# Performance work log

Measured on AMD Instinct MI355X. Metric: run time of the kernel, lower is better.

The kernel has to match this reference:

```python
import jax, jax.numpy as jnp
import numpy as np

B, N, K, OUT = 8, 2048, 30, 13


def _knn_idx(x, k):
    # x: [B,N,F] -> indices of k nearest neighbors (squared L2, includes self)
    sq = jnp.sum(x * x, axis=-1)  # [B,N]
    d = sq[:, :, None] + sq[:, None, :] - 2.0 * jnp.einsum('bnf,bmf->bnm', x, x)
    _, idx = jax.lax.top_k(-d, k)  # [B,N,k]
    return idx


def _edge_conv(x, W1, b1, g, be, W2, b2, k):
    # DynamicEdgeConv: kNN on feature space, message = MLP([x_i, x_j - x_i]), max aggr
    idx = _knn_idx(x, k)                                  # [B,N,k] (non-differentiable)
    xj = jax.vmap(lambda xb, ib: xb[ib])(x, idx)          # gather neighbors [B,N,k,F]
    xi = x[:, :, None, :]
    e = jnp.concatenate([jnp.broadcast_to(xi, xj.shape), xj - xi], axis=-1)  # [B,N,k,2F]
    # PyG MLP([2F,64,64]): Linear + BN(eval: affine) + ReLU, then plain Linear
    h = jax.nn.relu((e @ W1 + b1) * g + be)
    h = h @ W2 + b2
    return jnp.max(h, axis=2)                             # max over k neighbors -> [B,N,64]


def setup_inputs():
    key = jax.random.key(0)
    ks = jax.random.split(key, 40)

    def lin(i, fin, fout):
        W = jax.random.normal(ks[i], (fin, fout), jnp.float32) / np.sqrt(fin)
        return W, jnp.zeros((fout,), jnp.float32)

    inp = {}
    inp['x'] = jax.random.normal(ks[0], (B, N, 3), jnp.float32)
    inp['pos'] = jax.random.normal(ks[1], (B, N, 3), jnp.float32)
    inp['batch'] = jnp.repeat(jnp.arange(B, dtype=jnp.int32), N)
    i = 2
    for name, fin in [('c1', 12), ('c2', 128), ('c3', 128)]:
        W1, b1 = lin(i, fin, 64); i += 1
        W2, b2 = lin(i, 64, 64); i += 1
        inp[name + '_W1'] = W1; inp[name + '_b1'] = b1
        inp[name + '_g'] = 1.0 + 0.1 * jax.random.normal(ks[i], (64,), jnp.float32); i += 1
        inp[name + '_be'] = 0.1 * jax.random.normal(ks[i], (64,), jnp.float32); i += 1
        inp[name + '_W2'] = W2; inp[name + '_b2'] = b2
    dims = [192, 1024, 256, 128, OUT]
    for j in range(4):
        W, b = lin(i, dims[j], dims[j + 1]); i += 1
        inp[f'm_W{j + 1}'] = W; inp[f'm_b{j + 1}'] = b
    return inp


def reference(x, pos, batch,
              c1_W1, c1_b1, c1_g, c1_be, c1_W2, c1_b2,
              c2_W1, c2_b1, c2_g, c2_be, c2_W2, c2_b2,
              c3_W1, c3_b1, c3_g, c3_be, c3_W2, c3_b2,
              m_W1, m_b1, m_W2, m_b2, m_W3, m_b3, m_W4, m_b4):
    x0 = jnp.concatenate([pos, x], axis=-1)               # [B,N,6]
    x1 = _edge_conv(x0, c1_W1, c1_b1, c1_g, c1_be, c1_W2, c1_b2, K)
    x2 = _edge_conv(x1, c2_W1, c2_b1, c2_g, c2_be, c2_W2, c2_b2, K)
    x3 = _edge_conv(x2, c3_W1, c3_b1, c3_g, c3_be, c3_W2, c3_b2, K)
    h = jnp.concatenate([x1, x2, x3], axis=-1)            # [B,N,192]
    # classifier MLP([192,1024,256,128,OUT], norm=None): Linear+ReLU(+dropout=eval id), plain last
    h = jax.nn.relu(h @ m_W1 + m_b1)
    h = jax.nn.relu(h @ m_W2 + m_b2)
    h = jax.nn.relu(h @ m_W3 + m_b3)
    out = h @ m_W4 + m_b4
    return jax.nn.log_softmax(out, axis=-1), x3
```

## Files before the change

### kernel.cpp

```cpp
#include <hip/hip_runtime.h>

using u16 = unsigned short;
using u32 = unsigned int;
typedef short s8v __attribute__((ext_vector_type(8)));
typedef float f4v __attribute__((ext_vector_type(4)));

#define DEV static __device__ __forceinline__

DEV void cvt_split(float f, u16& h, u16& l) {
  u32 x = __builtin_bit_cast(u32, f);
  u32 rh = (x + 0x7FFFu + ((x >> 16) & 1u)) & 0xFFFF0000u;
  h = (u16)(rh >> 16);
  float fl = f - __builtin_bit_cast(float, rh);
  u32 y = __builtin_bit_cast(u32, fl);
  l = (u16)((y + 0x7FFFu + ((y >> 16) & 1u)) >> 16);
}

__global__ void k_misc0(const float* __restrict__ x, const float* __restrict__ pos,
                        float* __restrict__ x0, float* __restrict__ sq,
                        const float* __restrict__ W2c3, u16* __restrict__ eW2h, u16* __restrict__ eW2l) {
  int b = blockIdx.x;
  if (b < 64) {
    int p = b * 256 + threadIdx.x;
    float* o = x0 + (size_t)p * 8;
    float o0 = pos[p*3+0], o1 = pos[p*3+1], o2 = pos[p*3+2];
    float o3 = x[p*3+0],   o4 = x[p*3+1],   o5 = x[p*3+2];
    o[0] = o0; o[1] = o1; o[2] = o2;
    o[3] = o3; o[4] = o4; o[5] = o5;
    o[6] = 0.f; o[7] = 0.f;
    float s = ((o0*o0 + o4*o4) + (o2*o2 + 0.f)) + ((o1*o1 + o5*o5) + (o3*o3 + 0.f));
    sq[p] = s;
  } else {
    int e = (b - 64) * 256 + threadIdx.x;
    int k = e >> 6, n = e & 63;
    u16 h, l;
    cvt_split(W2c3[e], h, l);
    eW2h[n*72 + k] = h;
    eW2l[n*72 + k] = l;
  }
}

__global__ void k_splitmlp(const float* __restrict__ W1, const float* __restrict__ W2,
                           const float* __restrict__ W3,
                           u16* __restrict__ m1h, u16* __restrict__ m1l,
                           u16* __restrict__ m2h, u16* __restrict__ m2l,
                           u16* __restrict__ m3h, u16* __restrict__ m3l) {
  int b = blockIdx.x;
  u16 h, l;
  if (b < 768) {
    int e = b * 256 + threadIdx.x;
    if (e < 192 * 1024) {
      int k = e >> 10, n = e & 1023;
      cvt_split(W1[e], h, l);
      m1h[(size_t)n*200 + k] = h; m1l[(size_t)n*200 + k] = l;
    }
  } else if (b < 1792) {
    int e = (b - 768) * 256 + threadIdx.x;
    int k = e >> 8, n = e & 255;
    cvt_split(W2[e], h, l);
    m2h[(size_t)n*1032 + k] = h; m2l[(size_t)n*1032 + k] = l;
  } else {
    int e = (b - 1792) * 256 + threadIdx.x;
    int k = e >> 7, n = e & 127;
    cvt_split(W3[e], h, l);
    m3h[(size_t)n*264 + k] = h; m3l[(size_t)n*264 + k] = l;
  }
}

__global__ void k_splita(const float* __restrict__ A, u16* __restrict__ Ah, u16* __restrict__ Al) {
  int e = blockIdx.x * 256 + threadIdx.x;
  u16 h, l;
  cvt_split(A[e], h, l);
  Ah[e] = h; Al[e] = l;
}

template<int F>
__global__ __launch_bounds__(256, 2) void k_dist(const float* __restrict__ x, int stride,
    const float* __restrict__ sq, int cbase, float* __restrict__ D) {
  constexpr int PAD = F + 4;
  __shared__ __align__(16) float Xi[128 * PAD];
  __shared__ __align__(16) float Xj[128 * PAD];
  __shared__ float SQI[128], SQJ[128];
  int b  = blockIdx.z;
  int i0 = cbase + blockIdx.y * 128;
  int j0 = blockIdx.x * 128;
  int tid = threadIdx.x;
  constexpr int NPASS = 128 * (F / 4) / 256;
  #pragma unroll
  for (int ps = 0; ps < NPASS; ++ps) {
    int e4 = ps * 256 + tid;
    int r = e4 / (F / 4), f4 = (e4 % (F / 4)) * 4;
    *(float4*)&Xi[r*PAD + f4] = *(const float4*)&x[(size_t)(b*2048 + i0 + r)*stride + f4];
    *(float4*)&Xj[r*PAD + f4] = *(const float4*)&x[(size_t)(b*2048 + j0 + r)*stride + f4];
  }
  if (tid < 128) {
    SQI[tid] = sq[b*2048 + i0 + tid];
    SQJ[tid] = sq[b*2048 + j0 + tid];
  }
  __syncthreads();
  int tx = tid & 15, ty = tid >> 4;
  float acc[8][8];
  #pragma unroll
  for (int i = 0; i < 8; ++i)
    #pragma unroll
    for (int j = 0; j < 8; ++j) acc[i][j] = 0.f;
  #pragma unroll 2
  for (int kf = 0; kf < F; kf += 4) {
    float4 av[8], wv[8];
    #pragma unroll
    for (int i = 0; i < 8; ++i) av[i] = *(const float4*)&Xi[(ty + 16*i)*PAD + kf];
    #pragma unroll
    for (int j = 0; j < 8; ++j) wv[j] = *(const float4*)&Xj[(tx + 16*j)*PAD + kf];
    #pragma unroll
    for (int i = 0; i < 8; ++i)
      #pragma unroll
      for (int j = 0; j < 8; ++j) {
        acc[i][j] += av[i].x * wv[j].x;
        acc[i][j] += av[i].y * wv[j].y;
        acc[i][j] += av[i].z * wv[j].z;
        acc[i][j] += av[i].w * wv[j].w;
      }
  }
  #pragma unroll
  for (int i = 0; i < 8; ++i) {
    int row = ty + 16*i;
    float si = SQI[row];
    #pragma unroll
    for (int j = 0; j < 8; ++j) {
      int col = tx + 16*j;
      D[(size_t)(b*512 + blockIdx.y*128 + row)*2048 + j0 + col] =
          si + SQJ[col] - 2.f * acc[i][j];
    }
  }
}

__global__ __launch_bounds__(256) void k_topk(const float* __restrict__ D, int cbase,
                                              int* __restrict__ knn) {
  int wid  = blockIdx.x * 4 + (threadIdx.x >> 6);
  int lane = threadIdx.x & 63;
  int b = wid >> 9, il = wid & 511;
  const float* row = D + (size_t)(b*512 + il) * 2048;
  float v[32];
  #pragma unroll
  for (int s = 0; s < 32; ++s) v[s] = row[lane + 64*s];
  const float INFV = __builtin_bit_cast(float, 0x7f800000u);
  int wj = 0;
  #pragma unroll 1
  for (int it = 0; it < 30; ++it) {
    float mv = v[0]; int ms = 0;
    #pragma unroll
    for (int s = 1; s < 32; ++s) {
      bool lt = v[s] < mv;
      mv = lt ? v[s] : mv;
      ms = lt ? s : ms;
    }
    int mj = lane + (ms << 6);
    #pragma unroll
    for (int m = 1; m < 64; m <<= 1) {
      float ov = __shfl_xor(mv, m);
      int   oj = __shfl_xor(mj, m);
      bool take = (ov < mv) || ((ov == mv) && (oj < mj));
      mv = take ? ov : mv;
      mj = take ? oj : mj;
    }
    int gj = __builtin_amdgcn_readfirstlane(mj);
    if (lane == it) wj = gj;
    int owner = gj & 63, slot = gj >> 6;
    #pragma unroll
    for (int s = 0; s < 32; ++s) {
      if (slot == s) {
        if (lane == owner) v[s] = INFV;
      }
    }
  }
  if (lane < 30) knn[(size_t)(b*2048 + cbase + il)*30 + lane] = b*2048 + wj;
}

__global__ __launch_bounds__(256, 4) void k_prep(const float* __restrict__ x, int stride, int F,
    const float* __restrict__ W1, const float* __restrict__ b1,
    float* __restrict__ A0, float* __restrict__ V) {
  int p = blockIdx.x * 4 + (threadIdx.x >> 6);
  int lane = threadIdx.x & 63;
  float u = 0.f, v = 0.f;
  for (int f = 0; f < F; ++f) {
    float xv = x[(size_t)p*stride + f];
    float wa = W1[f*64 + lane];
    float wb = W1[(F + f)*64 + lane];
    u += xv * (wa - wb);
    v += xv * wb;
  }
  A0[p*64 + lane] = u + b1[lane];
  V[p*64 + lane]  = v;
}

__global__ __launch_bounds__(256, 3) void k_edge_b(const float* __restrict__ A0,
    const float* __restrict__ V, const int* __restrict__ knn,
    const float* __restrict__ W2, const float* __restrict__ b2,
    const float* __restrict__ g, const float* __restrict__ be,
    float* __restrict__ out, int ostride, float* __restrict__ sqout) {
  __shared__ __align__(16) float h1s[4][30][68];
  int wave = threadIdx.x >> 6, lane = threadIdx.x & 63;
  int p = blockIdx.x * 4 + wave;

  float a0 = A0[(size_t)p*64 + lane];
  float gg = g[lane], bbe = be[lane];
  const int* kr = knn + (size_t)p*30;

  #pragma unroll 2
  for (int k = 0; k < 30; ++k) {
    int j = kr[k];
    float v = V[(size_t)j*64 + lane];
    float pre = (a0 + v) * gg + bbe;
    h1s[wave][k][lane] = pre > 0.f ? pre : 0.f;
  }

  float w2c[64];
  #pragma unroll
  for (int c = 0; c < 64; ++c) w2c[c] = W2[c*64 + lane];

  float m = -3.0e38f;
  #pragma unroll 1
  for (int k = 0; k < 30; ++k) {
    float s0 = 0.f, s1 = 0.f, s2 = 0.f, s3 = 0.f;
    #pragma unroll
    for (int c = 0; c < 64; c += 4) {
      float4 hv = *(const float4*)&h1s[wave][k][c];
      s0 += hv.x * w2c[c+0];
      s1 += hv.y * w2c[c+1];
      s2 += hv.z * w2c[c+2];
      s3 += hv.w * w2c[c+3];
    }
    float h2 = (s0 + s1) + (s2 + s3);
    m = m > h2 ? m : h2;
  }
  float ov = m + b2[lane];
  out[(size_t)p*ostride + lane] = ov;

  float s = ov * ov;
  #pragma unroll
  for (int mm = 32; mm; mm >>= 1) s += __shfl_xor(s, mm);
  if (lane == 0) sqout[p] = s;
}

__global__ __launch_bounds__(256) void k_edge_m(const float* __restrict__ A0,
    const float* __restrict__ V, const int* __restrict__ knn,
    const u16* __restrict__ W2h, const u16* __restrict__ W2l,
    const float* __restrict__ b2,
    const float* __restrict__ g, const float* __restrict__ be,
    float* __restrict__ out, int ostride) {
  constexpr int PKW = 72;
  int p = blockIdx.x * 4 + (threadIdx.x >> 6);
  int lane = threadIdx.x & 63;
  int lr = lane & 15, kb = lane >> 4;

  const int* kr = knn + (size_t)p * 30;
  int j0 = kr[lr];
  int j1 = kr[lr + 16 < 30 ? lr + 16 : 29];

  s8v bh[4][2], bl[4][2];
  #pragma unroll
  for (int jf = 0; jf < 4; ++jf) {
    int n = jf*16 + lr;
    #pragma unroll
    for (int ks = 0; ks < 2; ++ks) {
      bh[jf][ks] = *(const s8v*)&W2h[n*PKW + ks*32 + kb*8];
      bl[jf][ks] = *(const s8v*)&W2l[n*PKW + ks*32 + kb*8];
    }
  }

  float base[2][8], gs[2][8];
  #pragma unroll
  for (int ks = 0; ks < 2; ++ks) {
    int cb = ks*32 + kb*8;
    float4 a0 = *(const float4*)&A0[(size_t)p*64 + cb];
    float4 a1 = *(const float4*)&A0[(size_t)p*64 + cb + 4];
    float4 g0 = *(const float4*)&g[cb];
    float4 g1 = *(const float4*)&g[cb + 4];
    float4 e0 = *(const float4*)&be[cb];
    float4 e1 = *(const float4*)&be[cb + 4];
    base[ks][0]=a0.x*g0.x+e0.x; base[ks][1]=a0.y*g0.y+e0.y;
    base[ks][2]=a0.z*g0.z+e0.z; base[ks][3]=a0.w*g0.w+e0.w;
    base[ks][4]=a1.x*g1.x+e1.x; base[ks][5]=a1.y*g1.y+e1.y;
    base[ks][6]=a1.z*g1.z+e1.z; base[ks][7]=a1.w*g1.w+e1.w;
    gs[ks][0]=g0.x; gs[ks][1]=g0.y; gs[ks][2]=g0.z; gs[ks][3]=g0.w;
    gs[ks][4]=g1.x; gs[ks][5]=g1.y; gs[ks][6]=g1.z; gs[ks][7]=g1.w;
  }

  s8v ah[2][2], al[2][2];
  #pragma unroll
  for (int mt = 0; mt < 2; ++mt) {
    const float* vr = V + (size_t)(mt ? j1 : j0) * 64;
    #pragma unroll
    for (int ks = 0; ks < 2; ++ks) {
      int cb = ks*32 + kb*8;
      float4 v0 = *(const float4*)&vr[cb];
      float4 v1 = *(const float4*)&vr[cb + 4];
      float hv[8];
      hv[0]=base[ks][0]+v0.x*gs[ks][0]; hv[1]=base[ks][1]+v0.y*gs[ks][1];
      hv[2]=base[ks][2]+v0.z*gs[ks][2]; hv[3]=base[ks][3]+v0.w*gs[ks][3];
      hv[4]=base[ks][4]+v1.x*gs[ks][4]; hv[5]=base[ks][5]+v1.y*gs[ks][5];
      hv[6]=base[ks][6]+v1.z*gs[ks][6]; hv[7]=base[ks][7]+v1.w*gs[ks][7];
      s8v hfrag, lfrag;
      #pragma unroll
      for (int e = 0; e < 8; ++e) {
        float h1 = hv[e] > 0.f ? hv[e] : 0.f;
        u16 hh, ll;
        cvt_split(h1, hh, ll);
        hfrag[e] = (short)hh; lfrag[e] = (short)ll;
      }
      ah[mt][ks] = hfrag; al[mt][ks] = lfrag;
    }
  }

  f4v acc[2][4];
  #pragma unroll
  for (int mt = 0; mt < 2; ++mt)
    #pragma unroll
    for (int jf = 0; jf < 4; ++jf) acc[mt][jf] = (f4v)(0.f);

  #pragma unroll
  for (int mt = 0; mt < 2; ++mt)
    #pragma unroll
    for (int jf = 0; jf < 4; ++jf)
      #pragma unroll
      for (int ks = 0; ks < 2; ++ks) {
        acc[mt][jf] = __builtin_amdgcn_mfma_f32_16x16x32_bf16(ah[mt][ks], bh[jf][ks], acc[mt][jf], 0, 0, 0);
        acc[mt][jf] = __builtin_amdgcn_mfma_f32_16x16x32_bf16(ah[mt][ks], bl[jf][ks], acc[mt][jf], 0, 0, 0);
        acc[mt][jf] = __builtin_amdgcn_mfma_f32_16x16x32_bf16(al[mt][ks], bh[jf][ks], acc[mt][jf], 0, 0, 0);
      }

  #pragma unroll
  for (int jf = 0; jf < 4; ++jf) {
    float m = fmaxf(fmaxf(acc[0][jf][0], acc[0][jf][1]), fmaxf(acc[0][jf][2], acc[0][jf][3]));
    float m1 = fmaxf(fmaxf(acc[1][jf][0], acc[1][jf][1]), fmaxf(acc[1][jf][2], acc[1][jf][3]));
    m = fmaxf(m, m1);
    m = fmaxf(m, __shfl_xor(m, 16));
    m = fmaxf(m, __shfl_xor(m, 32));
    if (kb == 0) out[(size_t)p*ostride + jf*16 + lr] = m + b2[jf*16 + lr];
  }
}

template<int NJF, int SPLIT>
__global__ __launch_bounds__(256) void k_mlp(
    const u16* __restrict__ Ahg, const u16* __restrict__ Alg, int lka,
    const u16* __restrict__ Wth, const u16* __restrict__ Wtl, int PKW,
    const float* __restrict__ bg,
    float* __restrict__ Cf, u16* __restrict__ Ch, u16* __restrict__ Cl,
    int ldc, int K) {
  int tid  = threadIdx.x;
  int wave = tid >> 6, lane = tid & 63;
  int wm = (wave >> 1) * 64, wn = (wave & 1) * (NJF*16);
  int lr = lane & 15, kb = lane >> 4;
  int m0 = blockIdx.y * 128, n0 = blockIdx.x * (2*NJF*16);

  f4v acc[4][NJF];
  #pragma unroll
  for (int i = 0; i < 4; ++i)
    #pragma unroll
    for (int j = 0; j < NJF; ++j) acc[i][j] = (f4v)(0.f);

  for (int k0 = 0; k0 < K; k0 += 32) {
    s8v bh[NJF], bl[NJF], ah[4], al[4];
    #pragma unroll
    for (int jf = 0; jf < NJF; ++jf) {
      int n = n0 + wn + jf*16 + lr;
      bh[jf] = *(const s8v*)&Wth[(size_t)n*PKW + k0 + kb*8];
      bl[jf] = *(const s8v*)&Wtl[(size_t)n*PKW + k0 + kb*8];
    }
    #pragma unroll
    for (int mf = 0; mf < 4; ++mf) {
      size_t a = (size_t)(m0 + wm + mf*16 + lr)*lka + k0 + kb*8;
      ah[mf] = *(const s8v*)&Ahg[a];
      al[mf] = *(const s8v*)&Alg[a];
    }
    #pragma unroll
    for (int mf = 0; mf < 4; ++mf)
      #pragma unroll
      for (int jf = 0; jf < NJF; ++jf) {
        acc[mf][jf] = __builtin_amdgcn_mfma_f32_16x16x32_bf16(ah[mf], bh[jf], acc[mf][jf], 0, 0, 0);
        acc[mf][jf] = __builtin_amdgcn_mfma_f32_16x16x32_bf16(ah[mf], bl[jf], acc[mf][jf], 0, 0, 0);
        acc[mf][jf] = __builtin_amdgcn_mfma_f32_16x16x32_bf16(al[mf], bh[jf], acc[mf][jf], 0, 0, 0);
      }
  }

  #pragma unroll
  for (int jf = 0; jf < NJF; ++jf) {
    int n = n0 + wn + jf*16 + lr;
    float bb = bg[n];
    #pragma unroll
    for (int mf = 0; mf < 4; ++mf) {
      #pragma unroll
      for (int r = 0; r < 4; ++r) {
        int m = m0 + wm + mf*16 + kb*4 + r;
        float v = acc[mf][jf][r] + bb;
        v = v > 0.f ? v : 0.f;
        if (SPLIT) {
          u16 h, l;
          cvt_split(v, h, l);
          Ch[(size_t)m*ldc + n] = h;
          Cl[(size_t)m*ldc + n] = l;
        } else {
          Cf[(size_t)m*ldc + n] = v;
        }
      }
    }
  }
}

__global__ __launch_bounds__(256) void k_head(const float* __restrict__ H3,
    const float* __restrict__ W4, const float* __restrict__ b4,
    float* __restrict__ out0, int pbase) {
  __shared__ float w4s[128 * 13];
  __shared__ float b4s[13];
  for (int e = threadIdx.x; e < 128*13; e += 256) w4s[e] = W4[e];
  if (threadIdx.x < 13) b4s[threadIdx.x] = b4[threadIdx.x];
  __syncthreads();
  int pl = blockIdx.x * 256 + threadIdx.x;
  float acc[13];
  #pragma unroll
  for (int c = 0; c < 13; ++c) acc[c] = b4s[c];
  const float* hr = H3 + (size_t)pl * 128;
  #pragma unroll 1
  for (int k = 0; k < 128; k += 4) {
    float4 h = *(const float4*)&hr[k];
    #pragma unroll
    for (int c = 0; c < 13; ++c) {
      acc[c] += h.x * w4s[(k+0)*13 + c];
      acc[c] += h.y * w4s[(k+1)*13 + c];
      acc[c] += h.z * w4s[(k+2)*13 + c];
      acc[c] += h.w * w4s[(k+3)*13 + c];
    }
  }
  float mx = acc[0];
  #pragma unroll
  for (int c = 1; c < 13; ++c) mx = fmaxf(mx, acc[c]);
  float s = 0.f;
  #pragma unroll
  for (int c = 0; c < 13; ++c) s += expf(acc[c] - mx);
  float lg = logf(s);
  size_t ob = (size_t)(pbase + pl) * 13;
  #pragma unroll
  for (int c = 0; c < 13; ++c) out0[ob + c] = acc[c] - mx - lg;
}

__global__ void k_out1(const float* __restrict__ hcat, float* __restrict__ out1) {
  int e = blockIdx.x * 256 + threadIdx.x;
  int p = e >> 6, c = e & 63;
  out1[e] = hcat[(size_t)p*192 + 128 + c];
}

extern "C" void kernel_launch(void* const* d_in, const int* in_sizes, int n_in,
                              void* d_out, int out_size, void* d_ws, size_t ws_size,
                              hipStream_t stream) {
  (void)in_sizes; (void)n_in; (void)out_size; (void)ws_size;
  const float* x   = (const float*)d_in[0];
  const float* pos = (const float*)d_in[1];
  const float* cw[3][6];
  for (int c = 0; c < 3; ++c)
    for (int t = 0; t < 6; ++t)
      cw[c][t] = (const float*)d_in[3 + c*6 + t];
  const float *mW[4], *mb[4];
  for (int j = 0; j < 4; ++j) {
    mW[j] = (const float*)d_in[21 + 2*j];
    mb[j] = (const float*)d_in[22 + 2*j];
  }

  float* ws   = (float*)d_ws;
  float* x0   = ws;
  float* sq   = x0 + 131072;
  int*   knn  = (int*)(sq + 16384);
  float* A0   = (float*)(knn + 491520);
  float* V    = A0 + 1048576;
  float* hcat = V + 1048576;
  float* U    = hcat + 3145728;
  float* H2c  = U + 8388608;
  float* H3c  = H2c + 2097152;
  u16*   eW2  = (u16*)(H3c + 1048576);

  u16* mwp = (u16*)(V + 524288);
  u16* m1h = mwp;            u16* m1l = m1h + 204800;
  u16* m2h = m1l + 204800;   u16* m2l = m2h + 264192;
  u16* m3h = m2l + 264192;   u16* m3l = m3h + 33792;
  u16* Aih = (u16*)A0;
  u16* Ail = Aih + 1572864;
  u16* H1h = (u16*)U;        u16* H1l = H1h + 8388608;
  u16* H2h = (u16*)H2c;      u16* H2l = H2h + 2097152;

  float* out0 = (float*)d_out;
  float* out1 = out0 + 8*2048*13;

  k_misc0<<<80, 256, 0, stream>>>(x, pos, x0, sq, cw[2][4], eW2, eW2 + 4608);

  for (int c = 0; c < 3; ++c) {
    const float* xin; int stride, F;
    if (c == 0)      { xin = x0;        stride = 8;   F = 6;  }
    else if (c == 1) { xin = hcat;      stride = 192; F = 64; }
    else             { xin = hcat + 64; stride = 192; F = 64; }
    for (int ch = 0; ch < 4; ++ch) {
      if (c == 0) k_dist<8> <<<dim3(16,4,8), 256, 0, stream>>>(xin, stride, sq, ch*512, U);
      else        k_dist<64><<<dim3(16,4,8), 256, 0, stream>>>(xin, stride, sq, ch*512, U);
      k_topk<<<1024, 256, 0, stream>>>(U, ch*512, knn);
    }
    k_prep<<<4096, 256, 0, stream>>>(xin, stride, F, cw[c][0], cw[c][1], A0, V);
    if (c < 2)
      k_edge_b<<<4096, 256, 0, stream>>>(A0, V, knn, cw[c][4], cw[c][5],
                                         cw[c][2], cw[c][3], hcat + 64*c, 192, sq);
    else
      k_edge_m<<<4096, 256, 0, stream>>>(A0, V, knn, eW2, eW2 + 4608,
                                         cw[c][5], cw[c][2], cw[c][3], hcat + 64*c, 192);
  }

  k_splitmlp<<<1920, 256, 0, stream>>>(mW[0], mW[1], mW[2], m1h, m1l, m2h, m2l, m3h, m3l);

  for (int ch = 0; ch < 2; ++ch) {
    k_splita<<<6144, 256, 0, stream>>>(hcat + (size_t)ch * 8192 * 192, Aih, Ail);
    k_mlp<4,1><<<dim3(8,64), 256, 0, stream>>>(Aih, Ail, 192,  m1h, m1l, 200,  mb[0],
                                               nullptr, H1h, H1l, 1024, 192);
    k_mlp<2,1><<<dim3(4,64), 256, 0, stream>>>(H1h, H1l, 1024, m2h, m2l, 1032, mb[1],
                                               nullptr, H2h, H2l, 256, 1024);
    k_mlp<2,0><<<dim3(2,64), 256, 0, stream>>>(H2h, H2l, 256,  m3h, m3l, 264,  mb[2],
                                               H3c, nullptr, nullptr, 128, 256);
    k_head<<<32, 256, 0, stream>>>(H3c, mW[3], mb[3], out0, ch*8192);
  }
  k_out1<<<4096, 256, 0, stream>>>(hcat, out1);
}
```

Baseline: 1.447 ms.

## Chunk k_dist feature loads, drop launch bound hints, precompute W1 difference

```diff
diff --git a/kernel.cpp b/kernel.cpp
--- a/kernel.cpp
+++ b/kernel.cpp
@@ -18,7 +18,10 @@
 
 __global__ void k_misc0(const float* __restrict__ x, const float* __restrict__ pos,
                         float* __restrict__ x0, float* __restrict__ sq,
-                        const float* __restrict__ W2c3, u16* __restrict__ eW2h, u16* __restrict__ eW2l) {
+                        const float* __restrict__ W2c3, u16* __restrict__ eW2h, u16* __restrict__ eW2l,
+                        const float* __restrict__ W1c1, const float* __restrict__ W1c2,
+                        const float* __restrict__ W1c3,
+                        float* __restrict__ wd1, float* __restrict__ wd2, float* __restrict__ wd3) {
   int b = blockIdx.x;
   if (b < 64) {
     int p = b * 256 + threadIdx.x;
@@ -30,13 +33,19 @@
     o[6] = 0.f; o[7] = 0.f;
     float s = ((o0*o0 + o4*o4) + (o2*o2 + 0.f)) + ((o1*o1 + o5*o5) + (o3*o3 + 0.f));
     sq[p] = s;
-  } else {
+  } else if (b < 80) {
     int e = (b - 64) * 256 + threadIdx.x;
     int k = e >> 6, n = e & 63;
     u16 h, l;
     cvt_split(W2c3[e], h, l);
     eW2h[n*72 + k] = h;
     eW2l[n*72 + k] = l;
+  } else if (b == 80) {
+    for (int e = threadIdx.x; e < 6*64; e += 256) wd1[e] = W1c1[e] - W1c1[6*64 + e];
+  } else if (b == 81) {
+    for (int e = threadIdx.x; e < 64*64; e += 256) wd2[e] = W1c2[e] - W1c2[64*64 + e];
+  } else {
+    for (int e = threadIdx.x; e < 64*64; e += 256) wd3[e] = W1c3[e] - W1c3[64*64 + e];
   }
 }
 
@@ -75,9 +84,10 @@
 }
 
 template<int F>
-__global__ __launch_bounds__(256, 2) void k_dist(const float* __restrict__ x, int stride,
+__global__ __launch_bounds__(256) void k_dist(const float* __restrict__ x, int stride,
     const float* __restrict__ sq, int cbase, float* __restrict__ D) {
-  constexpr int PAD = F + 4;
+  constexpr int BK = (F > 32) ? 32 : F;
+  constexpr int PAD = BK + 4;
   __shared__ __align__(16) float Xi[128 * PAD];
   __shared__ __align__(16) float Xj[128 * PAD];
   __shared__ float SQI[128], SQJ[128];
@@ -85,41 +95,45 @@
   int i0 = cbase + blockIdx.y * 128;
   int j0 = blockIdx.x * 128;
   int tid = threadIdx.x;
-  constexpr int NPASS = 128 * (F / 4) / 256;
-  #pragma unroll
-  for (int ps = 0; ps < NPASS; ++ps) {
-    int e4 = ps * 256 + tid;
-    int r = e4 / (F / 4), f4 = (e4 % (F / 4)) * 4;
-    *(float4*)&Xi[r*PAD + f4] = *(const float4*)&x[(size_t)(b*2048 + i0 + r)*stride + f4];
-    *(float4*)&Xj[r*PAD + f4] = *(const float4*)&x[(size_t)(b*2048 + j0 + r)*stride + f4];
-  }
   if (tid < 128) {
     SQI[tid] = sq[b*2048 + i0 + tid];
     SQJ[tid] = sq[b*2048 + j0 + tid];
   }
-  __syncthreads();
   int tx = tid & 15, ty = tid >> 4;
   float acc[8][8];
   #pragma unroll
   for (int i = 0; i < 8; ++i)
     #pragma unroll
     for (int j = 0; j < 8; ++j) acc[i][j] = 0.f;
-  #pragma unroll 2
-  for (int kf = 0; kf < F; kf += 4) {
-    float4 av[8], wv[8];
-    #pragma unroll
-    for (int i = 0; i < 8; ++i) av[i] = *(const float4*)&Xi[(ty + 16*i)*PAD + kf];
-    #pragma unroll
-    for (int j = 0; j < 8; ++j) wv[j] = *(const float4*)&Xj[(tx + 16*j)*PAD + kf];
-    #pragma unroll
-    for (int i = 0; i < 8; ++i)
-      #pragma unroll
-      for (int j = 0; j < 8; ++j) {
-        acc[i][j] += av[i].x * wv[j].x;
-        acc[i][j] += av[i].y * wv[j].y;
-        acc[i][j] += av[i].z * wv[j].z;
-        acc[i][j] += av[i].w * wv[j].w;
-      }
+
+  for (int kc = 0; kc < F; kc += BK) {
+    if (kc) __syncthreads();
+    constexpr int NPASS = 128 * (BK / 4) / 256;
+    #pragma unroll
+    for (int ps = 0; ps < NPASS; ++ps) {
+      int e4 = ps * 256 + tid;
+      int r = e4 / (BK / 4), f4 = (e4 % (BK / 4)) * 4;
+      *(float4*)&Xi[r*PAD + f4] = *(const float4*)&x[(size_t)(b*2048 + i0 + r)*stride + kc + f4];
+      *(float4*)&Xj[r*PAD + f4] = *(const float4*)&x[(size_t)(b*2048 + j0 + r)*stride + kc + f4];
+    }
+    __syncthreads();
+    #pragma unroll 2
+    for (int kf = 0; kf < BK; kf += 4) {
+      float4 av[8], wv[8];
+      #pragma unroll
+      for (int i = 0; i < 8; ++i) av[i] = *(const float4*)&Xi[(ty + 16*i)*PAD + kf];
+      #pragma unroll
+      for (int j = 0; j < 8; ++j) wv[j] = *(const float4*)&Xj[(tx + 16*j)*PAD + kf];
+      #pragma unroll
+      for (int i = 0; i < 8; ++i)
+        #pragma unroll
+        for (int j = 0; j < 8; ++j) {
+          acc[i][j] += av[i].x * wv[j].x;
+          acc[i][j] += av[i].y * wv[j].y;
+          acc[i][j] += av[i].z * wv[j].z;
+          acc[i][j] += av[i].w * wv[j].w;
+        }
+    }
   }
   #pragma unroll
   for (int i = 0; i < 8; ++i) {
@@ -177,23 +191,23 @@
 }
 
 __global__ __launch_bounds__(256, 4) void k_prep(const float* __restrict__ x, int stride, int F,
-    const float* __restrict__ W1, const float* __restrict__ b1,
+    const float* __restrict__ Wd, const float* __restrict__ W1, const float* __restrict__ b1,
     float* __restrict__ A0, float* __restrict__ V) {
   int p = blockIdx.x * 4 + (threadIdx.x >> 6);
   int lane = threadIdx.x & 63;
   float u = 0.f, v = 0.f;
   for (int f = 0; f < F; ++f) {
     float xv = x[(size_t)p*stride + f];
-    float wa = W1[f*64 + lane];
+    float wd = Wd[f*64 + lane];
     float wb = W1[(F + f)*64 + lane];
-    u += xv * (wa - wb);
+    u += xv * wd;
     v += xv * wb;
   }
   A0[p*64 + lane] = u + b1[lane];
   V[p*64 + lane]  = v;
 }
 
-__global__ __launch_bounds__(256, 3) void k_edge_b(const float* __restrict__ A0,
+__global__ __launch_bounds__(256) void k_edge_b(const float* __restrict__ A0,
     const float* __restrict__ V, const int* __restrict__ knn,
     const float* __restrict__ W2, const float* __restrict__ b2,
     const float* __restrict__ g, const float* __restrict__ be,
@@ -202,6 +216,10 @@
   int wave = threadIdx.x >> 6, lane = threadIdx.x & 63;
   int p = blockIdx.x * 4 + wave;
 
+  float w2c[64];
+  #pragma unroll
+  for (int c = 0; c < 64; ++c) w2c[c] = W2[c*64 + lane];
+
   float a0 = A0[(size_t)p*64 + lane];
   float gg = g[lane], bbe = be[lane];
   const int* kr = knn + (size_t)p*30;
@@ -213,10 +231,6 @@
     float pre = (a0 + v) * gg + bbe;
     h1s[wave][k][lane] = pre > 0.f ? pre : 0.f;
   }
-
-  float w2c[64];
-  #pragma unroll
-  for (int c = 0; c < 64; ++c) w2c[c] = W2[c*64 + lane];
 
   float m = -3.0e38f;
   #pragma unroll 1
@@ -476,6 +490,9 @@
   float* H2c  = U + 8388608;
   float* H3c  = H2c + 2097152;
   u16*   eW2  = (u16*)(H3c + 1048576);
+  float* wd1  = (float*)(eW2 + 9216);
+  float* wd2  = wd1 + 384;
+  float* wd3  = wd2 + 4096;
 
   u16* mwp = (u16*)(V + 524288);
   u16* m1h = mwp;            u16* m1l = m1h + 204800;
@@ -489,19 +506,20 @@
   float* out0 = (float*)d_out;
   float* out1 = out0 + 8*2048*13;
 
-  k_misc0<<<80, 256, 0, stream>>>(x, pos, x0, sq, cw[2][4], eW2, eW2 + 4608);
+  k_misc0<<<83, 256, 0, stream>>>(x, pos, x0, sq, cw[2][4], eW2, eW2 + 4608,
+                                  cw[0][0], cw[1][0], cw[2][0], wd1, wd2, wd3);
 
   for (int c = 0; c < 3; ++c) {
-    const float* xin; int stride, F;
-    if (c == 0)      { xin = x0;        stride = 8;   F = 6;  }
-    else if (c == 1) { xin = hcat;      stride = 192; F = 64; }
-    else             { xin = hcat + 64; stride = 192; F = 64; }
+    const float* xin; const float* wdc; int stride, F;
+    if (c == 0)      { xin = x0;        wdc = wd1; stride = 8;   F = 6;  }
+    else if (c == 1) { xin = hcat;      wdc = wd2; stride = 192; F = 64; }
+    else             { xin = hcat + 64; wdc = wd3; stride = 192; F = 64; }
     for (int ch = 0; ch < 4; ++ch) {
       if (c == 0) k_dist<8> <<<dim3(16,4,8), 256, 0, stream>>>(xin, stride, sq, ch*512, U);
       else        k_dist<64><<<dim3(16,4,8), 256, 0, stream>>>(xin, stride, sq, ch*512, U);
       k_topk<<<1024, 256, 0, stream>>>(U, ch*512, knn);
     }
-    k_prep<<<4096, 256, 0, stream>>>(xin, stride, F, cw[c][0], cw[c][1], A0, V);
+    k_prep<<<4096, 256, 0, stream>>>(xin, stride, F, wdc, cw[c][0], cw[c][1], A0, V);
     if (c < 2)
       k_edge_b<<<4096, 256, 0, stream>>>(A0, V, knn, cw[c][4], cw[c][5],
                                          cw[c][2], cw[c][3], hcat + 64*c, 192, sq);
```

Result: no change. 1.453 ms (+0.4%).
